# Kernel tuning notes

Measured on AMD Instinct MI355X. Metric: run time of the kernel, lower is better.

Reference implementation:

```python
import jax, jax.numpy as jnp
import numpy as np

B, N, D = 2, 4096, 256
H = 8
HD = D // H  # head dim = 32
DFF = 4 * D


def _layer_norm(x):
    # Matches source: (x - mean) / (std + 1e-6), std is population std (ddof=0)
    m = jnp.mean(x, axis=-1, keepdims=True)
    s = jnp.std(x, axis=-1, keepdims=True)
    return (x - m) / (s + 1e-6)


def setup_inputs() -> dict:
    key = jax.random.key(0)
    ks = jax.random.split(key, 11)
    sd = 1.0 / np.sqrt(D)
    sf = 1.0 / np.sqrt(DFF)
    return {
        "embeddings_in": jax.random.normal(ks[0], (B, N, D), dtype=jnp.float32),
        "Wq": jax.random.normal(ks[1], (D, D), dtype=jnp.float32) * sd,
        "bq": jnp.zeros((D,), dtype=jnp.float32),
        "Wk": jax.random.normal(ks[2], (D, D), dtype=jnp.float32) * sd,
        "bk": jnp.zeros((D,), dtype=jnp.float32),
        "Wv": jax.random.normal(ks[3], (D, D), dtype=jnp.float32) * sd,
        "bv": jnp.zeros((D,), dtype=jnp.float32),
        "Wo": jax.random.normal(ks[4], (D, D), dtype=jnp.float32) * sd,
        "bo": jnp.zeros((D,), dtype=jnp.float32),
        "W1": jax.random.normal(ks[5], (D, DFF), dtype=jnp.float32) * sd,
        "b1": jnp.zeros((DFF,), dtype=jnp.float32),
        "W2": jax.random.normal(ks[6], (DFF, D), dtype=jnp.float32) * sf,
        "b2": jnp.zeros((D,), dtype=jnp.float32),
    }


def reference(embeddings_in, Wq, bq, Wk, bk, Wv, bv, Wo, bo, W1, b1, W2, b2):
    x = embeddings_in
    xn1 = _layer_norm(x)
    # QKV projections, split into heads: [B,N,D] -> [B,H,N,HD]
    def heads(t):
        return jnp.transpose(t.reshape(B, N, H, HD), (0, 2, 1, 3))
    q = heads(xn1 @ Wq + bq)
    k = heads(xn1 @ Wk + bk)
    v = heads(xn1 @ Wv + bv)
    scores = jnp.einsum('bhnd,bhmd->bhnm', q, k) / jnp.sqrt(jnp.float32(HD))
    attn = jax.nn.softmax(scores, axis=-1)
    heads_out = jnp.einsum('bhnm,bhmd->bhnd', attn, v)
    attn_out = jnp.transpose(heads_out, (0, 2, 1, 3)).reshape(B, N, D)
    attn_out = attn_out @ Wo + bo  # dropout is identity in eval
    x_skip = attn_out + x
    xn2 = _layer_norm(x_skip)
    mlp = jax.nn.gelu(xn2 @ W1 + b1) @ W2 + b2
    return mlp + x_skip
```

## Files before the change

kernel.cpp:

```cpp
#include <hip/hip_runtime.h>
#include <hip/hip_bf16.h>

#define Bb 2
#define Nn 4096
#define Dd 256
#define Hh 8
#define HDh 32
#define DFFd 1024
#define MT (Bb*Nn)
#define Tt ((size_t)MT * Dd)
#define SPLIT 4
#define KVB (Nn / SPLIT)
#define NSTP (KVB / 64)

typedef __attribute__((ext_vector_type(8))) short short8;
typedef __attribute__((ext_vector_type(4))) float f32x4;
typedef __attribute__((address_space(1))) const unsigned int gu32;
typedef __attribute__((address_space(3))) unsigned int lu32;

__device__ __forceinline__ void gll16(const ushort* g, ushort* l) {
  __builtin_amdgcn_global_load_lds((gu32*)g, (lu32*)l, 16, 0, 0);
}
__device__ __forceinline__ float bf2f(ushort u){
  union { unsigned int i; float f; } v; v.i = ((unsigned int)u) << 16; return v.f;
}
__device__ __forceinline__ ushort f2bf(float f){
  union { float f; unsigned int i; } v; v.f = f;
  unsigned int r = v.i + 0x7fffu + ((v.i >> 16) & 1u);
  return (ushort)(r >> 16);
}
__device__ __forceinline__ int ars(int r){ return r * 64 + (r >> 3) * 32; }

__global__ __launch_bounds__(256) void prep_kernel(
    const float* __restrict__ Wq, const float* __restrict__ Wk,
    const float* __restrict__ Wv, const float* __restrict__ Wo,
    const float* __restrict__ W1, const float* __restrict__ W2,
    const float* __restrict__ bq, const float* __restrict__ bk,
    const float* __restrict__ bv, ushort* __restrict__ wt,
    float* __restrict__ bqkv)
{
  const int bid = blockIdx.x, t = threadIdx.x;
  if (bid == 192) {
    bqkv[t] = bq[t]; bqkv[256 + t] = bk[t]; bqkv[512 + t] = bv[t];
    return;
  }
  __shared__ __align__(16) ushort T[64][72];
  const float* src; ushort* dst; int Nsrc, Kdst, kt, nt;
  if (bid < 64) {
    const int m = bid >> 4, tile = bid & 15;
    kt = tile >> 2; nt = tile & 3; Nsrc = 256; Kdst = 256;
    src = (m == 0 ? Wq : m == 1 ? Wk : m == 2 ? Wv : Wo);
    dst = (m == 3) ? (wt + 196608) : (wt + m * 65536);
  } else if (bid < 128) {
    const int tile = bid - 64; kt = tile >> 4; nt = tile & 15;
    Nsrc = 1024; Kdst = 256; src = W1; dst = wt + 262144;
  } else {
    const int tile = bid - 128; kt = tile >> 2; nt = tile & 3;
    Nsrc = 256; Kdst = 1024; src = W2; dst = wt + 524288;
  }
  const int k0 = kt * 64, n0 = nt * 64;
  const int cc = t & 15, rr = t >> 4;
  #pragma unroll
  for (int pass = 0; pass < 4; pass++) {
    const int k = rr + pass * 16;
    const float4 v = *(const float4*)(src + (size_t)(k0 + k) * Nsrc + n0 + cc * 4);
    T[cc * 4 + 0][k] = f2bf(v.x); T[cc * 4 + 1][k] = f2bf(v.y);
    T[cc * 4 + 2][k] = f2bf(v.z); T[cc * 4 + 3][k] = f2bf(v.w);
  }
  __syncthreads();
  const int nl = t >> 2, ks = (t & 3) * 16;
  const short8 a = *(const short8*)(&T[nl][ks]);
  const short8 b = *(const short8*)(&T[nl][ks + 8]);
  ushort* drow = dst + (size_t)(n0 + nl) * Kdst + k0 + ks;
  *(short8*)(drow) = a; *(short8*)(drow + 8) = b;
}

__global__ __launch_bounds__(256) void ln_kernel(const float* __restrict__ x,
                                                 ushort* __restrict__ out)
{
  const int wave = threadIdx.x >> 6, lane = threadIdx.x & 63;
  const int row = blockIdx.x * 4 + wave;
  const float4 u = *(const float4*)(x + (size_t)row * Dd + lane * 4);
  float s1 = u.x + u.y + u.z + u.w;
  float s2 = u.x*u.x + u.y*u.y + u.z*u.z + u.w*u.w;
  #pragma unroll
  for (int m = 1; m < 64; m <<= 1) { s1 += __shfl_xor(s1, m, 64); s2 += __shfl_xor(s2, m, 64); }
  const float mean = s1 * (1.0f / Dd);
  float var = s2 * (1.0f / Dd) - mean * mean;
  var = var < 0.f ? 0.f : var;
  const float inv = 1.0f / (sqrtf(var) + 1e-6f);
  ushort4 o;
  o.x = f2bf((u.x - mean) * inv); o.y = f2bf((u.y - mean) * inv);
  o.z = f2bf((u.z - mean) * inv); o.w = f2bf((u.w - mean) * inv);
  *(ushort4*)(out + (size_t)row * Dd + lane * 4) = o;
}

template<int EPI, int BM>
__global__ __launch_bounds__(256) void gemm_epi(
    const ushort* __restrict__ A, const ushort* __restrict__ BT,
    const float* __restrict__ bias, const float* __restrict__ res,
    void* __restrict__ outv, int N, int K)
{
  constexpr int MI = BM / 64;
  constexpr int AI = BM / 32;
  __shared__ __align__(16) ushort AsF[2][BM * 64 + (BM / 8) * 32];
  __shared__ __align__(16) ushort BsF[2][64 * 64 + 8 * 32];
  const int tid = threadIdx.x;
  const int wave = tid >> 6, lane = tid & 63;
  const int quad = lane >> 4, l15 = lane & 15;
  const int n0 = blockIdx.x * 64, m0 = blockIdx.y * BM;
  f32x4 acc[MI][4];
  #pragma unroll
  for (int mt = 0; mt < MI; mt++)
    #pragma unroll
    for (int nt = 0; nt < 4; nt++) acc[mt][nt] = (f32x4){0.f,0.f,0.f,0.f};
  const int srow = lane >> 3, scol = (lane & 7) * 8;
  const ushort* gA[AI];
  #pragma unroll
  for (int ai = 0; ai < AI; ai++)
    gA[ai] = A + (size_t)(m0 + ai * 32 + wave * 8 + srow) * K + scol;
  const ushort* gB[2];
  #pragma unroll
  for (int bi = 0; bi < 2; bi++)
    gB[bi] = BT + (size_t)(n0 + bi * 32 + wave * 8 + srow) * K + scol;
  int aoff[MI], boff[4];
  #pragma unroll
  for (int mt = 0; mt < MI; mt++) aoff[mt] = ars(wave * 16 * MI + mt * 16 + l15);
  #pragma unroll
  for (int nt = 0; nt < 4; nt++) boff[nt] = ars(nt * 16 + l15);
  #pragma unroll
  for (int ai = 0; ai < AI; ai++) gll16(gA[ai], &AsF[0][ars(ai * 32 + wave * 8)]);
  #pragma unroll
  for (int bi = 0; bi < 2; bi++) gll16(gB[bi], &BsF[0][ars(bi * 32 + wave * 8)]);
  __syncthreads();
  const int NC = K >> 6;
  int p = 0;
  for (int c = 0; c < NC; c++) {
    if (c + 1 < NC) {
      #pragma unroll
      for (int ai = 0; ai < AI; ai++)
        gll16(gA[ai] + (c + 1) * 64, &AsF[p ^ 1][ars(ai * 32 + wave * 8)]);
      #pragma unroll
      for (int bi = 0; bi < 2; bi++)
        gll16(gB[bi] + (c + 1) * 64, &BsF[p ^ 1][ars(bi * 32 + wave * 8)]);
    }
    #pragma unroll
    for (int kk = 0; kk < 2; kk++) {
      short8 af[MI];
      #pragma unroll
      for (int mt = 0; mt < MI; mt++)
        af[mt] = *(const short8*)(&AsF[p][aoff[mt] + kk * 32 + quad * 8]);
      #pragma unroll
      for (int nt = 0; nt < 4; nt++) {
        const short8 bf = *(const short8*)(&BsF[p][boff[nt] + kk * 32 + quad * 8]);
        #pragma unroll
        for (int mt = 0; mt < MI; mt++)
          acc[mt][nt] = __builtin_amdgcn_mfma_f32_16x16x32_bf16(af[mt], bf, acc[mt][nt], 0, 0, 0);
      }
    }
    __syncthreads();
    p ^= 1;
  }
  #pragma unroll
  for (int mt = 0; mt < MI; mt++) {
    const int row0 = m0 + wave * (16 * MI) + mt * 16 + quad * 4;
    #pragma unroll
    for (int nt = 0; nt < 4; nt++) {
      const int col = n0 + nt * 16 + l15;
      const float bv = bias[col];
      float c[4];
      #pragma unroll
      for (int i = 0; i < 4; i++) c[i] = acc[mt][nt][i] + bv;
      if (EPI == 0) {
        ushort* qkv = (ushort*)outv;
        const int w = col >> 8, cd = col & 255;
        const int h = cd >> 5, hd = cd & 31;
        const int b = row0 >> 12, n = row0 & (Nn - 1);
        if (w < 2) {
          const float sc2 = (w == 0) ? (1.4426950408889634f * 0.17677669529663687f) : 1.0f;
          ushort* dst = qkv + (size_t)w * Tt + ((size_t)((b * Hh + h) * Nn) + n) * HDh + hd;
          #pragma unroll
          for (int i = 0; i < 4; i++) dst[(size_t)i * HDh] = f2bf(c[i] * sc2);
        } else {
          ushort4 pk;
          pk.x = f2bf(c[0]); pk.y = f2bf(c[1]); pk.z = f2bf(c[2]); pk.w = f2bf(c[3]);
          *(ushort4*)(qkv + 2 * Tt + ((size_t)((b * Hh + h) * HDh + hd)) * Nn + n) = pk;
        }
      } else if (EPI == 1) {
        float* out = (float*)outv;
        #pragma unroll
        for (int i = 0; i < 4; i++) {
          const size_t idx = (size_t)(row0 + i) * N + col;
          out[idx] = c[i] + res[idx];
        }
      } else {
        ushort* out = (ushort*)outv;
        #pragma unroll
        for (int i = 0; i < 4; i++) {
          const float t = tanhf(0.7978845608028654f * (c[i] + 0.044715f * c[i] * c[i] * c[i]));
          out[(size_t)(row0 + i) * N + col] = f2bf(0.5f * c[i] * (1.0f + t));
        }
      }
    }
  }
}

__global__ __launch_bounds__(256, 4) void attn_kernel(
    const ushort* __restrict__ qp, const ushort* __restrict__ kp,
    const ushort* __restrict__ vtg, ushort* __restrict__ op0,
    ushort* __restrict__ op123, float* __restrict__ lp)
{
  __shared__ __align__(16) ushort Ks[2][64][32];
  __shared__ __align__(16) ushort Vt[2][32][72];
  __shared__ __align__(16) ushort Ps[4][64][40];
  const int tid = threadIdx.x;
  const int wave = tid >> 6, lane = tid & 63;
  const int quad = lane >> 4, l15 = lane & 15;
  const int qtb = blockIdx.x, bh = blockIdx.y, sp = blockIdx.z;
  const size_t base = (size_t)bh * Nn * HDh;
  const int q0 = qtb * 256 + wave * 64;
  short8 qf[4];
  #pragma unroll
  for (int qt = 0; qt < 4; qt++)
    qf[qt] = *(const short8*)(qp + base + (size_t)(q0 + qt * 16 + l15) * HDh + quad * 8);
  const int kv0 = sp * KVB;
  const ushort* kg = kp + base + (size_t)(kv0 + wave * 16 + (lane >> 2)) * HDh + (lane & 3) * 8;
  const int vr = tid >> 3, vc = (tid & 7) * 8;
  const ushort* vg = vtg + base + (size_t)vr * Nn + kv0 + vc;
  ushort* psw = &Ps[wave][0][0];
  f32x4 o[2][4], ol[4];
  #pragma unroll
  for (int qt = 0; qt < 4; qt++) {
    o[0][qt] = (f32x4){0,0,0,0}; o[1][qt] = (f32x4){0,0,0,0};
    ol[qt] = (f32x4){0,0,0,0};
  }
  const short one = (short)0x3F80;
  const short8 ones = {one,one,one,one,one,one,one,one};
  const f32x4 zero4 = {0,0,0,0};
  gll16(kg, &Ks[0][wave * 16][0]);
  int4 vreg = *(const int4*)vg;
  *(int4*)(&Vt[0][vr][vc]) = vreg;
  vreg = *(const int4*)(vg + 64);
  __syncthreads();
  #pragma unroll 2
  for (int step = 0; step < NSTP; step++) {
    const int p = step & 1;
    if (step + 1 < NSTP) {
      gll16(kg + (size_t)(step + 1) * 64 * HDh, &Ks[p ^ 1][wave * 16][0]);
      *(int4*)(&Vt[p ^ 1][vr][vc]) = vreg;
    }
    if (step + 2 < NSTP) vreg = *(const int4*)(vg + (size_t)(step + 2) * 64);
    #pragma unroll
    for (int half = 0; half < 2; half++) {
      #pragma unroll
      for (int nt2 = 0; nt2 < 2; nt2++) {
        const int nt = half * 2 + nt2;
        const short8 kf = *(const short8*)(&Ks[p][nt * 16 + l15][quad * 8]);
        #pragma unroll
        for (int qt = 0; qt < 4; qt++) {
          const f32x4 s = __builtin_amdgcn_mfma_f32_16x16x32_bf16(kf, qf[qt], zero4, 0, 0, 0);
          const float p0 = __builtin_amdgcn_exp2f(s[0]);
          const float p1 = __builtin_amdgcn_exp2f(s[1]);
          const float p2 = __builtin_amdgcn_exp2f(s[2]);
          const float p3 = __builtin_amdgcn_exp2f(s[3]);
          uint2 pk;
          pk.x = __builtin_amdgcn_perm(__float_as_uint(p1) + 0x8000u,
                                       __float_as_uint(p0) + 0x8000u, 0x07060302u);
          pk.y = __builtin_amdgcn_perm(__float_as_uint(p3) + 0x8000u,
                                       __float_as_uint(p2) + 0x8000u, 0x07060302u);
          *(uint2*)(psw + (qt * 16 + l15) * 40 + nt2 * 16 + quad * 4) = pk;
        }
      }
      __builtin_amdgcn_wave_barrier();
      const short8 v0 = *(const short8*)(&Vt[p][l15][half * 32 + quad * 8]);
      const short8 v1 = *(const short8*)(&Vt[p][16 + l15][half * 32 + quad * 8]);
      #pragma unroll
      for (int qt = 0; qt < 4; qt++) {
        const short8 pb = *(const short8*)(psw + (qt * 16 + l15) * 40 + quad * 8);
        o[0][qt] = __builtin_amdgcn_mfma_f32_16x16x32_bf16(v0, pb, o[0][qt], 0, 0, 0);
        o[1][qt] = __builtin_amdgcn_mfma_f32_16x16x32_bf16(v1, pb, o[1][qt], 0, 0, 0);
        ol[qt]   = __builtin_amdgcn_mfma_f32_16x16x32_bf16(ones, pb, ol[qt], 0, 0, 0);
      }
      __builtin_amdgcn_wave_barrier();
    }
    __syncthreads();
  }
  lp[(size_t)sp * (16 * Nn) + (size_t)bh * Nn + q0 + lane] = ol[lane >> 4][0];
  ushort* ob = (sp == 0 ? op0 : op123 + (size_t)(sp - 1) * (16 * (size_t)Nn * HDh));
  #pragma unroll
  for (int pass = 0; pass < 2; pass++) {
    #pragma unroll
    for (int qt2 = 0; qt2 < 2; qt2++) {
      const int qt = pass * 2 + qt2;
      #pragma unroll
      for (int dt = 0; dt < 2; dt++) {
        ushort4 pk;
        pk.x = f2bf(o[dt][qt][0]); pk.y = f2bf(o[dt][qt][1]);
        pk.z = f2bf(o[dt][qt][2]); pk.w = f2bf(o[dt][qt][3]);
        *(ushort4*)(psw + (qt2 * 16 + l15) * 40 + dt * 16 + quad * 4) = pk;
      }
    }
    __builtin_amdgcn_wave_barrier();
    #pragma unroll
    for (int j = 0; j < 2; j++) {
      const int row = j * 16 + (lane >> 2);
      const short8 ov = *(const short8*)(psw + row * 40 + (lane & 3) * 8);
      const int q = q0 + pass * 32 + row;
      *(short8*)(ob + ((size_t)bh * Nn + q) * HDh + (lane & 3) * 8) = ov;
    }
    __builtin_amdgcn_wave_barrier();
  }
}

__global__ __launch_bounds__(256) void attn_combine(
    const ushort* __restrict__ op0, const ushort* __restrict__ op123,
    const float* __restrict__ lp, ushort* __restrict__ attn)
{
  const int idx = blockIdx.x * 256 + threadIdx.x;
  const int d8 = idx & 3, n = (idx >> 2) & (Nn - 1), bh = idx >> 14;
  const size_t ln = (size_t)bh * Nn + n;
  float l = 0.f;
  #pragma unroll
  for (int sp = 0; sp < SPLIT; sp++) l += lp[(size_t)sp * (16 * Nn) + ln];
  const float inv = 1.0f / l;
  float acc[8];
  #pragma unroll
  for (int k = 0; k < 8; k++) acc[k] = 0.f;
  const size_t qoff = ln * HDh + d8 * 8;
  #pragma unroll
  for (int sp = 0; sp < SPLIT; sp++) {
    const ushort* src = (sp == 0 ? op0 : op123 + (size_t)(sp - 1) * (16 * (size_t)Nn * HDh)) + qoff;
    const short8 u = *(const short8*)src;
    #pragma unroll
    for (int k = 0; k < 8; k++) acc[k] += bf2f((ushort)u[k]);
  }
  short8 ov;
  #pragma unroll
  for (int k = 0; k < 8; k++) ov[k] = (short)f2bf(acc[k] * inv);
  const int b = bh >> 3, h = bh & 7;
  *(short8*)(attn + ((size_t)(b * Nn + n)) * Dd + h * HDh + d8 * 8) = ov;
}

extern "C" void kernel_launch(void* const* d_in, const int* in_sizes, int n_in,
                              void* d_out, int out_size, void* d_ws, size_t ws_size,
                              hipStream_t stream)
{
  const float* x  = (const float*)d_in[0];
  const float* Wq = (const float*)d_in[1];
  const float* bq = (const float*)d_in[2];
  const float* Wk = (const float*)d_in[3];
  const float* bk = (const float*)d_in[4];
  const float* Wv = (const float*)d_in[5];
  const float* bv = (const float*)d_in[6];
  const float* Wo = (const float*)d_in[7];
  const float* bo = (const float*)d_in[8];
  const float* W1 = (const float*)d_in[9];
  const float* b1 = (const float*)d_in[10];
  const float* W2 = (const float*)d_in[11];
  const float* b2 = (const float*)d_in[12];

  char* ws = (char*)d_ws;
  ushort* wt    = (ushort*)ws;
  ushort* wtqkv = wt;
  ushort* wto   = wt + 196608;
  ushort* wt1   = wt + 262144;
  ushort* wt2   = wt + 524288;
  float*  bqkv  = (float*)(ws + 786432 * 2);
  ushort* s0    = (ushort*)(ws + 786432 * 2 + 4096);
  ushort* s1    = s0 + Tt;
  ushort* s2    = s1 + Tt;
  ushort* s3    = s2 + Tt;
  float*  xsk   = (float*)(s3 + Tt);
  ushort* xn2   = (ushort*)(xsk + Tt);
  ushort* xn1   = s0;
  ushort* hid   = s0;
  ushort* op0   = s0;
  ushort* op123 = (ushort*)xsk;
  float*  lp    = (float*)d_out;
  ushort* attnb = (ushort*)((char*)d_out + (4u << 20));
  float*  outp  = (float*)d_out;

  const dim3 blk(256);
  hipLaunchKernelGGL(prep_kernel, dim3(193), blk, 0, stream,
                     Wq, Wk, Wv, Wo, W1, W2, bq, bk, bv, wt, bqkv);
  hipLaunchKernelGGL(ln_kernel, dim3(MT / 4), blk, 0, stream, x, xn1);
  hipLaunchKernelGGL((gemm_epi<0,128>), dim3(12, 64), blk, 0, stream,
                     xn1, wtqkv, bqkv, (const float*)nullptr, (void*)s1, 768, Dd);

  hipLaunchKernelGGL(attn_kernel, dim3(Nn / 256, Bb * Hh, SPLIT), blk, 0, stream,
                     s1, s2, s3, op0, op123, lp);
  hipLaunchKernelGGL(attn_combine, dim3((Bb * Hh * Nn * 4) / 256), blk, 0, stream,
                     op0, op123, lp, attnb);

  hipLaunchKernelGGL((gemm_epi<1,64>), dim3(4, 128), blk, 0, stream,
                     attnb, wto, bo, x, (void*)xsk, Dd, Dd);
  hipLaunchKernelGGL(ln_kernel, dim3(MT / 4), blk, 0, stream, xsk, xn2);
  hipLaunchKernelGGL((gemm_epi<2,128>), dim3(16, 64), blk, 0, stream,
                     xn2, wt1, b1, (const float*)nullptr, (void*)hid, DFFd, Dd);
  hipLaunchKernelGGL((gemm_epi<1,64>), dim3(4, 128), blk, 0, stream,
                     hid, wt2, b2, xsk, (void*)outp, Dd, DFFd);
}
```

Baseline: 201.6 us.

## Fuse all stages into one cooperative persistent kernel with grid syncs

Replaces the nine separate kernel launches with a single cooperative kernel of 512 blocks that runs prep, layernorm, QKV GEMM, attention, combine, Wo GEMM, layernorm and the two MLP GEMMs as phases separated by grid.sync. The attention KV split drops from 4 to 2 so the attention grid matches 512 blocks, and the combine step simplifies to two partials. The goal is to remove per-launch overhead and inter-kernel gaps. In exchange, the grid barriers add cost, occupancy is capped at 2 blocks per CU, the shared LDS buffer must fit the largest phase, and attention has less parallelism per block. If the cooperative launch fails, it falls back to separate launches.

```diff
diff --git a/kernel.cpp b/kernel.cpp
--- a/kernel.cpp
+++ b/kernel.cpp
@@ -1,5 +1,7 @@
 #include <hip/hip_runtime.h>
-#include <hip/hip_bf16.h>
+#include <hip/hip_cooperative_groups.h>
+
+namespace cg = cooperative_groups;
 
 #define Bb 2
 #define Nn 4096
@@ -9,7 +11,7 @@
 #define DFFd 1024
 #define MT (Bb*Nn)
 #define Tt ((size_t)MT * Dd)
-#define SPLIT 4
+#define SPLIT 2
 #define KVB (Nn / SPLIT)
 #define NSTP (KVB / 64)
 
@@ -31,84 +33,88 @@
 }
 __device__ __forceinline__ int ars(int r){ return r * 64 + (r >> 3) * 32; }
 
-__global__ __launch_bounds__(256) void prep_kernel(
-    const float* __restrict__ Wq, const float* __restrict__ Wk,
-    const float* __restrict__ Wv, const float* __restrict__ Wo,
-    const float* __restrict__ W1, const float* __restrict__ W2,
-    const float* __restrict__ bq, const float* __restrict__ bk,
-    const float* __restrict__ bv, ushort* __restrict__ wt,
-    float* __restrict__ bqkv)
-{
-  const int bid = blockIdx.x, t = threadIdx.x;
-  if (bid == 192) {
-    bqkv[t] = bq[t]; bqkv[256 + t] = bk[t]; bqkv[512 + t] = bv[t];
+struct KP {
+  const float *x,*Wq,*bq,*Wk,*bk,*Wv,*bv,*Wo,*bo,*W1,*b1,*W2,*b2;
+  ushort* wt; float* bqkv;
+  ushort *xn1, *qb;
+  ushort *op0, *op1; float* lp; ushort* attnb;
+  float* xsk; ushort* xn2; ushort* hid; float* outp;
+};
+
+__device__ __forceinline__ void prep_unit(ushort* LB, int unit, int tid, const KP& p)
+{
+  if (unit == 192) {
+    p.bqkv[tid] = p.bq[tid]; p.bqkv[256 + tid] = p.bk[tid]; p.bqkv[512 + tid] = p.bv[tid];
     return;
   }
-  __shared__ __align__(16) ushort T[64][72];
+  ushort* T = LB;
   const float* src; ushort* dst; int Nsrc, Kdst, kt, nt;
-  if (bid < 64) {
-    const int m = bid >> 4, tile = bid & 15;
+  if (unit < 64) {
+    const int m = unit >> 4, tile = unit & 15;
     kt = tile >> 2; nt = tile & 3; Nsrc = 256; Kdst = 256;
-    src = (m == 0 ? Wq : m == 1 ? Wk : m == 2 ? Wv : Wo);
-    dst = (m == 3) ? (wt + 196608) : (wt + m * 65536);
-  } else if (bid < 128) {
-    const int tile = bid - 64; kt = tile >> 4; nt = tile & 15;
-    Nsrc = 1024; Kdst = 256; src = W1; dst = wt + 262144;
+    src = (m == 0 ? p.Wq : m == 1 ? p.Wk : m == 2 ? p.Wv : p.Wo);
+    dst = (m == 3) ? (p.wt + 196608) : (p.wt + m * 65536);
+  } else if (unit < 128) {
+    const int tile = unit - 64; kt = tile >> 4; nt = tile & 15;
+    Nsrc = 1024; Kdst = 256; src = p.W1; dst = p.wt + 262144;
   } else {
-    const int tile = bid - 128; kt = tile >> 2; nt = tile & 3;
-    Nsrc = 256; Kdst = 1024; src = W2; dst = wt + 524288;
+    const int tile = unit - 128; kt = tile >> 2; nt = tile & 3;
+    Nsrc = 256; Kdst = 1024; src = p.W2; dst = p.wt + 524288;
   }
   const int k0 = kt * 64, n0 = nt * 64;
-  const int cc = t & 15, rr = t >> 4;
+  const int cc = tid & 15, rr = tid >> 4;
   #pragma unroll
   for (int pass = 0; pass < 4; pass++) {
     const int k = rr + pass * 16;
     const float4 v = *(const float4*)(src + (size_t)(k0 + k) * Nsrc + n0 + cc * 4);
-    T[cc * 4 + 0][k] = f2bf(v.x); T[cc * 4 + 1][k] = f2bf(v.y);
-    T[cc * 4 + 2][k] = f2bf(v.z); T[cc * 4 + 3][k] = f2bf(v.w);
+    T[(cc * 4 + 0) * 72 + k] = f2bf(v.x); T[(cc * 4 + 1) * 72 + k] = f2bf(v.y);
+    T[(cc * 4 + 2) * 72 + k] = f2bf(v.z); T[(cc * 4 + 3) * 72 + k] = f2bf(v.w);
   }
   __syncthreads();
-  const int nl = t >> 2, ks = (t & 3) * 16;
-  const short8 a = *(const short8*)(&T[nl][ks]);
-  const short8 b = *(const short8*)(&T[nl][ks + 8]);
+  const int nl = tid >> 2, ks = (tid & 3) * 16;
+  const short8 a = *(const short8*)(&T[nl * 72 + ks]);
+  const short8 b = *(const short8*)(&T[nl * 72 + ks + 8]);
   ushort* drow = dst + (size_t)(n0 + nl) * Kdst + k0 + ks;
   *(short8*)(drow) = a; *(short8*)(drow + 8) = b;
 }
 
-__global__ __launch_bounds__(256) void ln_kernel(const float* __restrict__ x,
-                                                 ushort* __restrict__ out)
-{
-  const int wave = threadIdx.x >> 6, lane = threadIdx.x & 63;
-  const int row = blockIdx.x * 4 + wave;
-  const float4 u = *(const float4*)(x + (size_t)row * Dd + lane * 4);
-  float s1 = u.x + u.y + u.z + u.w;
-  float s2 = u.x*u.x + u.y*u.y + u.z*u.z + u.w*u.w;
-  #pragma unroll
-  for (int m = 1; m < 64; m <<= 1) { s1 += __shfl_xor(s1, m, 64); s2 += __shfl_xor(s2, m, 64); }
-  const float mean = s1 * (1.0f / Dd);
-  float var = s2 * (1.0f / Dd) - mean * mean;
-  var = var < 0.f ? 0.f : var;
-  const float inv = 1.0f / (sqrtf(var) + 1e-6f);
-  ushort4 o;
-  o.x = f2bf((u.x - mean) * inv); o.y = f2bf((u.y - mean) * inv);
-  o.z = f2bf((u.z - mean) * inv); o.w = f2bf((u.w - mean) * inv);
-  *(ushort4*)(out + (size_t)row * Dd + lane * 4) = o;
+__device__ __forceinline__ void ln_rows(const float* __restrict__ x,
+                                        ushort* __restrict__ out, int row0, int tid)
+{
+  const int wave = tid >> 6, lane = tid & 63;
+  #pragma unroll
+  for (int r = 0; r < 4; r++) {
+    const int row = row0 + wave * 4 + r;
+    const float4 u = *(const float4*)(x + (size_t)row * Dd + lane * 4);
+    float s1 = u.x + u.y + u.z + u.w;
+    float s2 = u.x*u.x + u.y*u.y + u.z*u.z + u.w*u.w;
+    #pragma unroll
+    for (int m = 1; m < 64; m <<= 1) { s1 += __shfl_xor(s1, m, 64); s2 += __shfl_xor(s2, m, 64); }
+    const float mean = s1 * (1.0f / Dd);
+    float var = s2 * (1.0f / Dd) - mean * mean;
+    var = var < 0.f ? 0.f : var;
+    const float inv = 1.0f / (sqrtf(var) + 1e-6f);
+    ushort4 o;
+    o.x = f2bf((u.x - mean) * inv); o.y = f2bf((u.y - mean) * inv);
+    o.z = f2bf((u.z - mean) * inv); o.w = f2bf((u.w - mean) * inv);
+    *(ushort4*)(out + (size_t)row * Dd + lane * 4) = o;
+  }
 }
 
 template<int EPI, int BM>
-__global__ __launch_bounds__(256) void gemm_epi(
-    const ushort* __restrict__ A, const ushort* __restrict__ BT,
+__device__ __forceinline__ void gemm_unit(
+    ushort* LB, const ushort* __restrict__ A, const ushort* __restrict__ BT,
     const float* __restrict__ bias, const float* __restrict__ res,
-    void* __restrict__ outv, int N, int K)
+    void* outv, int N, int K, int m0, int n0, int tid)
 {
   constexpr int MI = BM / 64;
   constexpr int AI = BM / 32;
-  __shared__ __align__(16) ushort AsF[2][BM * 64 + (BM / 8) * 32];
-  __shared__ __align__(16) ushort BsF[2][64 * 64 + 8 * 32];
-  const int tid = threadIdx.x;
+  constexpr int APL = BM * 64 + (BM / 8) * 32;
+  constexpr int BPL = 64 * 64 + 8 * 32;
+  ushort* AsF = LB;
+  ushort* BsF = LB + 2 * APL;
   const int wave = tid >> 6, lane = tid & 63;
   const int quad = lane >> 4, l15 = lane & 15;
-  const int n0 = blockIdx.x * 64, m0 = blockIdx.y * BM;
   f32x4 acc[MI][4];
   #pragma unroll
   for (int mt = 0; mt < MI; mt++)
@@ -129,9 +135,9 @@
   #pragma unroll
   for (int nt = 0; nt < 4; nt++) boff[nt] = ars(nt * 16 + l15);
   #pragma unroll
-  for (int ai = 0; ai < AI; ai++) gll16(gA[ai], &AsF[0][ars(ai * 32 + wave * 8)]);
-  #pragma unroll
-  for (int bi = 0; bi < 2; bi++) gll16(gB[bi], &BsF[0][ars(bi * 32 + wave * 8)]);
+  for (int ai = 0; ai < AI; ai++) gll16(gA[ai], AsF + ars(ai * 32 + wave * 8));
+  #pragma unroll
+  for (int bi = 0; bi < 2; bi++) gll16(gB[bi], BsF + ars(bi * 32 + wave * 8));
   __syncthreads();
   const int NC = K >> 6;
   int p = 0;
@@ -139,20 +145,20 @@
     if (c + 1 < NC) {
       #pragma unroll
       for (int ai = 0; ai < AI; ai++)
-        gll16(gA[ai] + (c + 1) * 64, &AsF[p ^ 1][ars(ai * 32 + wave * 8)]);
+        gll16(gA[ai] + (c + 1) * 64, AsF + (p ^ 1) * APL + ars(ai * 32 + wave * 8));
       #pragma unroll
       for (int bi = 0; bi < 2; bi++)
-        gll16(gB[bi] + (c + 1) * 64, &BsF[p ^ 1][ars(bi * 32 + wave * 8)]);
+        gll16(gB[bi] + (c + 1) * 64, BsF + (p ^ 1) * BPL + ars(bi * 32 + wave * 8));
     }
     #pragma unroll
     for (int kk = 0; kk < 2; kk++) {
       short8 af[MI];
       #pragma unroll
       for (int mt = 0; mt < MI; mt++)
-        af[mt] = *(const short8*)(&AsF[p][aoff[mt] + kk * 32 + quad * 8]);
+        af[mt] = *(const short8*)(AsF + p * APL + aoff[mt] + kk * 32 + quad * 8);
       #pragma unroll
       for (int nt = 0; nt < 4; nt++) {
-        const short8 bf = *(const short8*)(&BsF[p][boff[nt] + kk * 32 + quad * 8]);
+        const short8 bf = *(const short8*)(BsF + p * BPL + boff[nt] + kk * 32 + quad * 8);
         #pragma unroll
         for (int mt = 0; mt < MI; mt++)
           acc[mt][nt] = __builtin_amdgcn_mfma_f32_16x16x32_bf16(af[mt], bf, acc[mt][nt], 0, 0, 0);
@@ -205,18 +211,16 @@
   }
 }
 
-__global__ __launch_bounds__(256, 4) void attn_kernel(
-    const ushort* __restrict__ qp, const ushort* __restrict__ kp,
-    const ushort* __restrict__ vtg, ushort* __restrict__ op0,
-    ushort* __restrict__ op123, float* __restrict__ lp)
-{
-  __shared__ __align__(16) ushort Ks[2][64][32];
-  __shared__ __align__(16) ushort Vt[2][32][72];
-  __shared__ __align__(16) ushort Ps[4][64][40];
-  const int tid = threadIdx.x;
+__device__ __forceinline__ void attn_unit(
+    ushort* LB, const ushort* __restrict__ qp, const ushort* __restrict__ kp,
+    const ushort* __restrict__ vtg, ushort* op0, ushort* op1,
+    float* lp, int qtb, int bh, int sp, int tid)
+{
+  ushort* Ks = LB;
+  ushort* Vt = LB + 4096;
+  ushort* Ps = LB + 8704;
   const int wave = tid >> 6, lane = tid & 63;
   const int quad = lane >> 4, l15 = lane & 15;
-  const int qtb = blockIdx.x, bh = blockIdx.y, sp = blockIdx.z;
   const size_t base = (size_t)bh * Nn * HDh;
   const int q0 = qtb * 256 + wave * 64;
   short8 qf[4];
@@ -227,7 +231,7 @@
   const ushort* kg = kp + base + (size_t)(kv0 + wave * 16 + (lane >> 2)) * HDh + (lane & 3) * 8;
   const int vr = tid >> 3, vc = (tid & 7) * 8;
   const ushort* vg = vtg + base + (size_t)vr * Nn + kv0 + vc;
-  ushort* psw = &Ps[wave][0][0];
+  ushort* psw = Ps + wave * (64 * 40);
   f32x4 o[2][4], ol[4];
   #pragma unroll
   for (int qt = 0; qt < 4; qt++) {
@@ -237,17 +241,17 @@
   const short one = (short)0x3F80;
   const short8 ones = {one,one,one,one,one,one,one,one};
   const f32x4 zero4 = {0,0,0,0};
-  gll16(kg, &Ks[0][wave * 16][0]);
+  gll16(kg, Ks + (wave * 16) * 32);
   int4 vreg = *(const int4*)vg;
-  *(int4*)(&Vt[0][vr][vc]) = vreg;
+  *(int4*)(Vt + vr * 72 + vc) = vreg;
   vreg = *(const int4*)(vg + 64);
   __syncthreads();
   #pragma unroll 2
   for (int step = 0; step < NSTP; step++) {
     const int p = step & 1;
     if (step + 1 < NSTP) {
-      gll16(kg + (size_t)(step + 1) * 64 * HDh, &Ks[p ^ 1][wave * 16][0]);
-      *(int4*)(&Vt[p ^ 1][vr][vc]) = vreg;
+      gll16(kg + (size_t)(step + 1) * 64 * HDh, Ks + (p ^ 1) * 2048 + (wave * 16) * 32);
+      *(int4*)(Vt + (p ^ 1) * 2304 + vr * 72 + vc) = vreg;
     }
     if (step + 2 < NSTP) vreg = *(const int4*)(vg + (size_t)(step + 2) * 64);
     #pragma unroll
@@ -255,7 +259,7 @@
       #pragma unroll
       for (int nt2 = 0; nt2 < 2; nt2++) {
         const int nt = half * 2 + nt2;
-        const short8 kf = *(const short8*)(&Ks[p][nt * 16 + l15][quad * 8]);
+        const short8 kf = *(const short8*)(Ks + p * 2048 + (nt * 16 + l15) * 32 + quad * 8);
         #pragma unroll
         for (int qt = 0; qt < 4; qt++) {
           const f32x4 s = __builtin_amdgcn_mfma_f32_16x16x32_bf16(kf, qf[qt], zero4, 0, 0, 0);
@@ -272,8 +276,8 @@
         }
       }
       __builtin_amdgcn_wave_barrier();
-      const short8 v0 = *(const short8*)(&Vt[p][l15][half * 32 + quad * 8]);
-      const short8 v1 = *(const short8*)(&Vt[p][16 + l15][half * 32 + quad * 8]);
+      const short8 v0 = *(const short8*)(Vt + p * 2304 + l15 * 72 + half * 32 + quad * 8);
+      const short8 v1 = *(const short8*)(Vt + p * 2304 + (16 + l15) * 72 + half * 32 + quad * 8);
       #pragma unroll
       for (int qt = 0; qt < 4; qt++) {
         const short8 pb = *(const short8*)(psw + (qt * 16 + l15) * 40 + quad * 8);
@@ -286,7 +290,7 @@
     __syncthreads();
   }
   lp[(size_t)sp * (16 * Nn) + (size_t)bh * Nn + q0 + lane] = ol[lane >> 4][0];
-  ushort* ob = (sp == 0 ? op0 : op123 + (size_t)(sp - 1) * (16 * (size_t)Nn * HDh));
+  ushort* ob = (sp == 0 ? op0 : op1);
   #pragma unroll
   for (int pass = 0; pass < 2; pass++) {
     #pragma unroll
@@ -312,91 +316,145 @@
   }
 }
 
-__global__ __launch_bounds__(256) void attn_combine(
-    const ushort* __restrict__ op0, const ushort* __restrict__ op123,
-    const float* __restrict__ lp, ushort* __restrict__ attn)
-{
-  const int idx = blockIdx.x * 256 + threadIdx.x;
+__device__ __forceinline__ void combine_unit(
+    const ushort* __restrict__ op0, const ushort* __restrict__ op1,
+    const float* __restrict__ lp, ushort* __restrict__ attn, int unit, int tid)
+{
+  const int idx = unit * 256 + tid;
   const int d8 = idx & 3, n = (idx >> 2) & (Nn - 1), bh = idx >> 14;
   const size_t ln = (size_t)bh * Nn + n;
-  float l = 0.f;
-  #pragma unroll
-  for (int sp = 0; sp < SPLIT; sp++) l += lp[(size_t)sp * (16 * Nn) + ln];
-  const float inv = 1.0f / l;
-  float acc[8];
-  #pragma unroll
-  for (int k = 0; k < 8; k++) acc[k] = 0.f;
+  const float inv = 1.0f / (lp[ln] + lp[(size_t)(16 * Nn) + ln]);
   const size_t qoff = ln * HDh + d8 * 8;
-  #pragma unroll
-  for (int sp = 0; sp < SPLIT; sp++) {
-    const ushort* src = (sp == 0 ? op0 : op123 + (size_t)(sp - 1) * (16 * (size_t)Nn * HDh)) + qoff;
-    const short8 u = *(const short8*)src;
-    #pragma unroll
-    for (int k = 0; k < 8; k++) acc[k] += bf2f((ushort)u[k]);
-  }
+  const short8 a = *(const short8*)(op0 + qoff);
+  const short8 b = *(const short8*)(op1 + qoff);
   short8 ov;
   #pragma unroll
-  for (int k = 0; k < 8; k++) ov[k] = (short)f2bf(acc[k] * inv);
-  const int b = bh >> 3, h = bh & 7;
-  *(short8*)(attn + ((size_t)(b * Nn + n)) * Dd + h * HDh + d8 * 8) = ov;
+  for (int k = 0; k < 8; k++)
+    ov[k] = (short)f2bf((bf2f((ushort)a[k]) + bf2f((ushort)b[k])) * inv);
+  const int bb = bh >> 3, h = bh & 7;
+  *(short8*)(attn + ((size_t)(bb * Nn + n)) * Dd + h * HDh + d8 * 8) = ov;
+}
+
+__global__ __launch_bounds__(256, 2) void mega(KP p)
+{
+  cg::grid_group grid = cg::this_grid();
+  __shared__ __align__(16) ushort LB[26112];
+  const int gid = blockIdx.x, tid = threadIdx.x;
+  if (gid < 193) prep_unit(LB, gid, tid, p);
+  ln_rows(p.x, p.xn1, gid * 16, tid);
+  grid.sync();
+  for (int u = gid; u < 768; u += 512)
+    gemm_unit<0,128>(LB, p.xn1, p.wt, p.bqkv, nullptr, (void*)p.qb,
+                     768, 256, (u / 12) * 128, (u % 12) * 64, tid);
+  grid.sync();
+  {
+    const int bh = gid & 15, qtb = (gid >> 4) & 15, sp = gid >> 8;
+    attn_unit(LB, p.qb, p.qb + Tt, p.qb + 2 * Tt, p.op0, p.op1, p.lp, qtb, bh, sp, tid);
+  }
+  grid.sync();
+  #pragma unroll
+  for (int it = 0; it < 2; it++)
+    combine_unit(p.op0, p.op1, p.lp, p.attnb, gid + it * 512, tid);
+  grid.sync();
+  gemm_unit<1,64>(LB, p.attnb, p.wt + 196608, p.bo, p.x, (void*)p.xsk,
+                  256, 256, (gid >> 2) * 64, (gid & 3) * 64, tid);
+  grid.sync();
+  ln_rows(p.xsk, p.xn2, gid * 16, tid);
+  grid.sync();
+  for (int it = 0; it < 2; it++) {
+    const int u = gid + it * 512;
+    gemm_unit<2,128>(LB, p.xn2, p.wt + 262144, p.b1, nullptr, (void*)p.hid,
+                     1024, 256, (u >> 4) * 128, (u & 15) * 64, tid);
+  }
+  grid.sync();
+  gemm_unit<1,64>(LB, p.hid, p.wt + 524288, p.b2, p.xsk, (void*)p.outp,
+                  256, 1024, (gid >> 2) * 64, (gid & 3) * 64, tid);
+}
+
+__global__ __launch_bounds__(256) void k_p0(KP p){
+  __shared__ __align__(16) ushort LB[4608];
+  if (blockIdx.x < 193) prep_unit(LB, blockIdx.x, threadIdx.x, p);
+  ln_rows(p.x, p.xn1, blockIdx.x * 16, threadIdx.x);
+}
+__global__ __launch_bounds__(256) void k_qkv(KP p){
+  __shared__ __align__(16) ushort LB[26112];
+  for (int u = blockIdx.x; u < 768; u += 512)
+    gemm_unit<0,128>(LB, p.xn1, p.wt, p.bqkv, nullptr, (void*)p.qb,
+                     768, 256, (u / 12) * 128, (u % 12) * 64, threadIdx.x);
+}
+__global__ __launch_bounds__(256) void k_attn(KP p){
+  __shared__ __align__(16) ushort LB[18944];
+  const int gid = blockIdx.x;
+  attn_unit(LB, p.qb, p.qb + Tt, p.qb + 2 * Tt, p.op0, p.op1, p.lp,
+            (gid >> 4) & 15, gid & 15, gid >> 8, threadIdx.x);
+}
+__global__ __launch_bounds__(256) void k_comb(KP p){
+  for (int it = 0; it < 2; it++)
+    combine_unit(p.op0, p.op1, p.lp, p.attnb, blockIdx.x + it * 512, threadIdx.x);
+}
+__global__ __launch_bounds__(256) void k_wo(KP p){
+  __shared__ __align__(16) ushort LB[17408];
+  gemm_unit<1,64>(LB, p.attnb, p.wt + 196608, p.bo, p.x, (void*)p.xsk,
+                  256, 256, (blockIdx.x >> 2) * 64, (blockIdx.x & 3) * 64, threadIdx.x);
+}
+__global__ __launch_bounds__(256) void k_ln2(KP p){
+  ln_rows(p.xsk, p.xn2, blockIdx.x * 16, threadIdx.x);
+}
+__global__ __launch_bounds__(256) void k_w1(KP p){
+  __shared__ __align__(16) ushort LB[26112];
+  for (int it = 0; it < 2; it++) {
+    const int u = blockIdx.x + it * 512;
+    gemm_unit<2,128>(LB, p.xn2, p.wt + 262144, p.b1, nullptr, (void*)p.hid,
+                     1024, 256, (u >> 4) * 128, (u & 15) * 64, threadIdx.x);
+  }
+}
+__global__ __launch_bounds__(256) void k_w2(KP p){
+  __shared__ __align__(16) ushort LB[17408];
+  gemm_unit<1,64>(LB, p.hid, p.wt + 524288, p.b2, p.xsk, (void*)p.outp,
+                  256, 1024, (blockIdx.x >> 2) * 64, (blockIdx.x & 3) * 64, threadIdx.x);
 }
 
 extern "C" void kernel_launch(void* const* d_in, const int* in_sizes, int n_in,
                               void* d_out, int out_size, void* d_ws, size_t ws_size,
                               hipStream_t stream)
 {
-  const float* x  = (const float*)d_in[0];
-  const float* Wq = (const float*)d_in[1];
-  const float* bq = (const float*)d_in[2];
-  const float* Wk = (const float*)d_in[3];
-  const float* bk = (const float*)d_in[4];
-  const float* Wv = (const float*)d_in[5];
-  const float* bv = (const float*)d_in[6];
-  const float* Wo = (const float*)d_in[7];
-  const float* bo = (const float*)d_in[8];
-  const float* W1 = (const float*)d_in[9];
-  const float* b1 = (const float*)d_in[10];
-  const float* W2 = (const float*)d_in[11];
-  const float* b2 = (const float*)d_in[12];
+  KP p;
+  p.x  = (const float*)d_in[0];
+  p.Wq = (const float*)d_in[1];  p.bq = (const float*)d_in[2];
+  p.Wk = (const float*)d_in[3];  p.bk = (const float*)d_in[4];
+  p.Wv = (const float*)d_in[5];  p.bv = (const float*)d_in[6];
+  p.Wo = (const float*)d_in[7];  p.bo = (const float*)d_in[8];
+  p.W1 = (const float*)d_in[9];  p.b1 = (const float*)d_in[10];
+  p.W2 = (const float*)d_in[11]; p.b2 = (const float*)d_in[12];
 
   char* ws = (char*)d_ws;
-  ushort* wt    = (ushort*)ws;
-  ushort* wtqkv = wt;
-  ushort* wto   = wt + 196608;
-  ushort* wt1   = wt + 262144;
-  ushort* wt2   = wt + 524288;
-  float*  bqkv  = (float*)(ws + 786432 * 2);
-  ushort* s0    = (ushort*)(ws + 786432 * 2 + 4096);
-  ushort* s1    = s0 + Tt;
-  ushort* s2    = s1 + Tt;
-  ushort* s3    = s2 + Tt;
-  float*  xsk   = (float*)(s3 + Tt);
-  ushort* xn2   = (ushort*)(xsk + Tt);
-  ushort* xn1   = s0;
-  ushort* hid   = s0;
-  ushort* op0   = s0;
-  ushort* op123 = (ushort*)xsk;
-  float*  lp    = (float*)d_out;
-  ushort* attnb = (ushort*)((char*)d_out + (4u << 20));
-  float*  outp  = (float*)d_out;
-
-  const dim3 blk(256);
-  hipLaunchKernelGGL(prep_kernel, dim3(193), blk, 0, stream,
-                     Wq, Wk, Wv, Wo, W1, W2, bq, bk, bv, wt, bqkv);
-  hipLaunchKernelGGL(ln_kernel, dim3(MT / 4), blk, 0, stream, x, xn1);
-  hipLaunchKernelGGL((gemm_epi<0,128>), dim3(12, 64), blk, 0, stream,
-                     xn1, wtqkv, bqkv, (const float*)nullptr, (void*)s1, 768, Dd);
-
-  hipLaunchKernelGGL(attn_kernel, dim3(Nn / 256, Bb * Hh, SPLIT), blk, 0, stream,
-                     s1, s2, s3, op0, op123, lp);
-  hipLaunchKernelGGL(attn_combine, dim3((Bb * Hh * Nn * 4) / 256), blk, 0, stream,
-                     op0, op123, lp, attnb);
-
-  hipLaunchKernelGGL((gemm_epi<1,64>), dim3(4, 128), blk, 0, stream,
-                     attnb, wto, bo, x, (void*)xsk, Dd, Dd);
-  hipLaunchKernelGGL(ln_kernel, dim3(MT / 4), blk, 0, stream, xsk, xn2);
-  hipLaunchKernelGGL((gemm_epi<2,128>), dim3(16, 64), blk, 0, stream,
-                     xn2, wt1, b1, (const float*)nullptr, (void*)hid, DFFd, Dd);
-  hipLaunchKernelGGL((gemm_epi<1,64>), dim3(4, 128), blk, 0, stream,
-                     hid, wt2, b2, xsk, (void*)outp, Dd, DFFd);
-}
+  p.wt   = (ushort*)ws;
+  p.bqkv = (float*)(ws + 786432 * 2);
+  ushort* s0 = (ushort*)(ws + 786432 * 2 + 4096);
+  ushort* s1 = s0 + Tt;
+  p.xsk  = (float*)(s1 + 3 * Tt);
+  p.xn2  = (ushort*)(p.xsk + Tt);
+  p.xn1  = s0;
+  p.qb   = s1;
+  p.op0  = s0;
+  p.op1  = (ushort*)p.xsk;
+  p.lp   = (float*)d_out;
+  p.attnb= (ushort*)((char*)d_out + (4u << 20));
+  p.hid  = s0;
+  p.outp = (float*)d_out;
+
+  void* args[] = { (void*)&p };
+  hipError_t e = hipLaunchCooperativeKernel((const void*)mega, dim3(512), dim3(256),
+                                            args, 0, stream);
+  if (e != hipSuccess) {
+    const dim3 g(512), b(256);
+    hipLaunchKernelGGL(k_p0,   g, b, 0, stream, p);
+    hipLaunchKernelGGL(k_qkv,  g, b, 0, stream, p);
+    hipLaunchKernelGGL(k_attn, g, b, 0, stream, p);
+    hipLaunchKernelGGL(k_comb, g, b, 0, stream, p);
+    hipLaunchKernelGGL(k_wo,   g, b, 0, stream, p);
+    hipLaunchKernelGGL(k_ln2,  g, b, 0, stream, p);
+    hipLaunchKernelGGL(k_w1,   g, b, 0, stream, p);
+    hipLaunchKernelGGL(k_w2,   g, b, 0, stream, p);
+  }
+}
```

New measurement: 649.1 us. +221.9%, slower.
